# Performance work log

Measured on AMD Instinct MI355X. Metric: run time of the kernel, lower is better.

The kernel has to match this reference:

```python
import jax, jax.numpy as jnp
import numpy as np

B, V, C, M, CM, D, OUT = 16, 16, 64, 32, 16, 128, 600
VOCAB = {"cond": 4000, "proc": 2000, "drug": 600, "lab_item": 700, "lab_value": 2000, "inj_item": 400, "inj_value": 2000}


def _gru(x, Wih, Whh, bih, bhh):
    """Batch-first torch-style GRU. x: [N,T,D] -> (outputs [N,T,D], h_T [N,D])."""
    Dh = Whh.shape[1]

    def step(h, xt):
        gi = xt @ Wih.T + bih
        gh = h @ Whh.T + bhh
        ir, iz, ig = jnp.split(gi, 3, axis=-1)
        hr, hz, hg = jnp.split(gh, 3, axis=-1)
        r = jax.nn.sigmoid(ir + hr)
        z = jax.nn.sigmoid(iz + hz)
        n = jnp.tanh(ig + r * hg)
        h = (1.0 - z) * n + z * h
        return h, h

    h0 = jnp.zeros((x.shape[0], Dh), x.dtype)
    hT, ys = jax.lax.scan(step, h0, jnp.swapaxes(x, 0, 1))
    return jnp.swapaxes(ys, 0, 1), hT


def _hetero_mp(feats, Wself, Wmsg):
    """Heterogeneous message passing over node types on the fully-connected
    monitor<->visit-feature bipartite pattern: each node type combines a self
    transform with a transformed mean of the other node types, then ReLU.
    feats: list of [N,D]; Wself/Wmsg: [T,D,D]."""
    stacked = jnp.stack(feats)  # [T,N,D]
    total = jnp.sum(stacked, axis=0)
    T = stacked.shape[0]
    outs = []
    for t in range(T):
        others = (total - stacked[t]) / (T - 1)
        outs.append(jax.nn.relu(stacked[t] @ Wself[t] + others @ Wmsg[t]))
    return outs


def _forward(codes_cond, codes_proc, codes_drug, codes_lab_item, codes_lab_value,
             codes_inj_item, codes_inj_value, weight, age,
             emb_cond, emb_proc, emb_drug, emb_lab_item, emb_lab_value,
             emb_inj_item, emb_inj_value,
             mgru_Wih, mgru_Whh, mgru_bih, mgru_bhh,
             vgru_Wih, vgru_Whh, vgru_bih, vgru_bhh,
             gnn_Wself, gnn_Wmsg,
             fc_weight_W, fc_weight_b, fc_age_W, fc_age_b,
             fc_patient_W, fc_patient_b):
    # ---- visit-event features: embedding lookup + sum-pool over codes ----
    vis = {}
    for k, codes, emb in (("cond", codes_cond, emb_cond),
                          ("proc", codes_proc, emb_proc),
                          ("drug", codes_drug, emb_drug)):
        vis[k] = jnp.sum(emb[codes], axis=2)  # [B,V,D]
    visit_keys = ("cond", "proc", "drug")

    # ---- monitor-event pairs: (item * value) embeddings, GNN, two-level GRU ----
    pairs = (
        (codes_lab_item, codes_lab_value, emb_lab_item, emb_lab_value, "lab_item", (0, 2, 3, 4)),
        (codes_inj_item, codes_inj_value, emb_inj_item, emb_inj_value, "inj_item", (1, 2, 3, 4)),
    )
    hid = {}
    for p, (ci, cv, ei, ev, ikey, gidx) in enumerate(pairs):
        mon = jnp.sum(ei[ci] * ev[cv], axis=3)  # [B,V,M,D]
        feats = [mon.reshape(-1, D)]  # monitor node type, [B*V*M, D]
        for k in visit_keys:  # visit features repeated across monitors
            feats.append(jnp.broadcast_to(vis[k][:, :, None, :], (B, V, M, D)).reshape(-1, D))
        outs = _hetero_mp(feats, gnn_Wself[p], gnn_Wmsg[p])
        for t, k in enumerate((ikey,) + visit_keys):
            g = gidx[t]
            # monitor-level GRU over the M monitors of each visit
            o, _ = _gru(outs[t].reshape(B * V, M, D), mgru_Wih[g], mgru_Whh[g], mgru_bih[g], mgru_bhh[g])
            last = o[:, -1, :].reshape(B, V, D)  # last monitor state per visit
            # visit-level GRU (source uses visit_gru[feature_key1] for all keys)
            _, h = _gru(last, vgru_Wih[p], vgru_Whh[p], vgru_bih[p], vgru_bhh[p])
            hid[k] = h if k not in hid else hid[k] + h

    # ---- weight / age scalar features ----
    for k, x, W, b, vi in (("weight", weight, fc_weight_W, fc_weight_b, 2),
                           ("age", age, fc_age_W, fc_age_b, 3)):
        mask = (x != 0.0)[..., None]  # [B,V,1]
        xe = (x[..., None] * W[:, 0] + b) * mask  # Linear(1->D) then zero-mask
        _, h = _gru(xe, vgru_Wih[vi], vgru_Whh[vi], vgru_bih[vi], vgru_bhh[vi])
        hid[k] = h

    # ---- concat in dict-insertion order, then ReLU + Linear head ----
    pe = jnp.concatenate([hid["lab_item"], hid["cond"], hid["proc"], hid["drug"],
                          hid["inj_item"], hid["weight"], hid["age"]], axis=-1)  # [B, 7D]
    return jax.nn.relu(pe) @ fc_patient_W.T + fc_patient_b  # [B, OUT]


def setup_inputs() -> dict:
    key = jax.random.key(0)
    ks = iter(jax.random.split(key, 64))

    def nrm(shape, s=0.1):
        return (jax.random.normal(next(ks), shape) * s).astype(jnp.float32)

    def emb_table(vsz):
        t = nrm((vsz, D), 1.0)
        return t.at[0].set(0.0)  # padding_idx=0 row is zero

    inp = {}
    inp["codes_cond"] = jax.random.randint(next(ks), (B, V, C), 0, VOCAB["cond"], dtype=jnp.int32)
    inp["codes_proc"] = jax.random.randint(next(ks), (B, V, C), 0, VOCAB["proc"], dtype=jnp.int32)
    inp["codes_drug"] = jax.random.randint(next(ks), (B, V, C), 0, VOCAB["drug"], dtype=jnp.int32)
    inp["codes_lab_item"] = jax.random.randint(next(ks), (B, V, M, CM), 0, VOCAB["lab_item"], dtype=jnp.int32)
    inp["codes_lab_value"] = jax.random.randint(next(ks), (B, V, M, CM), 0, VOCAB["lab_value"], dtype=jnp.int32)
    inp["codes_inj_item"] = jax.random.randint(next(ks), (B, V, M, CM), 0, VOCAB["inj_item"], dtype=jnp.int32)
    inp["codes_inj_value"] = jax.random.randint(next(ks), (B, V, M, CM), 0, VOCAB["inj_value"], dtype=jnp.int32)
    inp["weight"] = jax.random.uniform(next(ks), (B, V), minval=0.1, maxval=1.0, dtype=jnp.float32)
    inp["age"] = jax.random.uniform(next(ks), (B, V), minval=0.1, maxval=1.0, dtype=jnp.float32)
    inp["emb_cond"] = emb_table(VOCAB["cond"])
    inp["emb_proc"] = emb_table(VOCAB["proc"])
    inp["emb_drug"] = emb_table(VOCAB["drug"])
    inp["emb_lab_item"] = emb_table(VOCAB["lab_item"])
    inp["emb_lab_value"] = emb_table(VOCAB["lab_value"])
    inp["emb_inj_item"] = emb_table(VOCAB["inj_item"])
    inp["emb_inj_value"] = emb_table(VOCAB["inj_value"])
    inp["mgru_Wih"] = nrm((5, 3 * D, D))
    inp["mgru_Whh"] = nrm((5, 3 * D, D))
    inp["mgru_bih"] = nrm((5, 3 * D))
    inp["mgru_bhh"] = nrm((5, 3 * D))
    inp["vgru_Wih"] = nrm((4, 3 * D, D))
    inp["vgru_Whh"] = nrm((4, 3 * D, D))
    inp["vgru_bih"] = nrm((4, 3 * D))
    inp["vgru_bhh"] = nrm((4, 3 * D))
    inp["gnn_Wself"] = nrm((2, 4, D, D))
    inp["gnn_Wmsg"] = nrm((2, 4, D, D))
    inp["fc_weight_W"] = nrm((D, 1))
    inp["fc_weight_b"] = nrm((D,))
    inp["fc_age_W"] = nrm((D, 1))
    inp["fc_age_b"] = nrm((D,))
    inp["fc_patient_W"] = nrm((OUT, 7 * D))
    inp["fc_patient_b"] = nrm((OUT,))
    return inp


def reference(codes_cond, codes_proc, codes_drug, codes_lab_item, codes_lab_value,
              codes_inj_item, codes_inj_value, weight, age,
              emb_cond, emb_proc, emb_drug, emb_lab_item, emb_lab_value,
              emb_inj_item, emb_inj_value,
              mgru_Wih, mgru_Whh, mgru_bih, mgru_bhh,
              vgru_Wih, vgru_Whh, vgru_bih, vgru_bhh,
              gnn_Wself, gnn_Wmsg,
              fc_weight_W, fc_weight_b, fc_age_W, fc_age_b,
              fc_patient_W, fc_patient_b):
    return _forward(codes_cond, codes_proc, codes_drug, codes_lab_item, codes_lab_value,
                    codes_inj_item, codes_inj_value, weight, age,
                    emb_cond, emb_proc, emb_drug, emb_lab_item, emb_lab_value,
                    emb_inj_item, emb_inj_value,
                    mgru_Wih, mgru_Whh, mgru_bih, mgru_bhh,
                    vgru_Wih, vgru_Whh, vgru_bih, vgru_bhh,
                    gnn_Wself, gnn_Wmsg,
                    fc_weight_W, fc_weight_b, fc_age_W, fc_age_b,
                    fc_patient_W, fc_patient_b)
```

## Files before the change

kernel.cpp:

```cpp
#include <hip/hip_runtime.h>
#include <math.h>

#define B_   16
#define V_   16
#define C_   64
#define M_   32
#define CM_  16
#define D_   128
#define OUT_ 600
#define NSEQ 256
#define NROW 8192

typedef __attribute__((ext_vector_type(8))) short bf16x8;
typedef __attribute__((ext_vector_type(4))) short bf16x4;
typedef __attribute__((ext_vector_type(4))) float f32x4;

__device__ __forceinline__ unsigned short f2bf(float x) {
  union { float f; unsigned u; } v; v.f = x;
  unsigned r = v.u + 0x7fff + ((v.u >> 16) & 1);
  return (unsigned short)(r >> 16);
}
__device__ __forceinline__ float bf2f(short s) {
  union { unsigned u; float f; } v;
  v.u = ((unsigned)(unsigned short)s) << 16;
  return v.f;
}
__device__ __forceinline__ float fsig(float x)  { return __fdividef(1.f, 1.f + __expf(-x)); }
__device__ __forceinline__ float ftanh(float x) { return 1.f - 2.f*__fdividef(1.f, __expf(2.f*x) + 1.f); }

constexpr int OFF_VIS   = 0;
constexpr int OFF_VISB  = 98304;
constexpr int OFF_MONB  = 147456;
constexpr int OFF_TOTB  = 1196032;
constexpr int OFF_W12T  = 2244608;
constexpr int OFF_WIHB  = 2375680;
constexpr int OFF_WIHTV = 2498560;
constexpr int OFF_XE    = 2695168;
constexpr int OFF_GI    = 2760704;
constexpr int OFF_LAST  = 27926528;
constexpr int OFF_VGI   = 28188672;
constexpr int OFF_VH    = 29171712;
constexpr int OFF_PE    = 29192192;

__global__ __launch_bounds__(256) void k_prep(
    const float* __restrict__ Wself, const float* __restrict__ Wmsg,
    const float* __restrict__ mWih,  const float* __restrict__ vWih,
    const float* __restrict__ wgt,   const float* __restrict__ age,
    const float* __restrict__ fwW,   const float* __restrict__ fwB,
    const float* __restrict__ faW,   const float* __restrict__ faB,
    short* __restrict__ w12t, short* __restrict__ wihb,
    float* __restrict__ wihTv, float* __restrict__ xe)
{
  int bx = blockIdx.x, tid = threadIdx.x;
  if (bx < 1024) {
    int lin = bx*256 + tid;
    int pt = lin >> 15, rem = lin & 32767;
    int n = rem >> 8, k = rem & 255;
    float v;
    if (k < 128) v = Wself[pt*16384 + k*128 + n] - Wmsg[pt*16384 + k*128 + n]*(1.f/3.f);
    else         v = Wmsg[pt*16384 + (k-128)*128 + n]*(1.f/3.f);
    w12t[lin] = (short)f2bf(v);
  } else if (bx < 1984) {
    int lin = (bx-1024)*256 + tid;
    wihb[lin] = (short)f2bf(mWih[lin]);
  } else if (bx < 2752) {
    int lin = (bx-1984)*256 + tid;
    int g = lin / 49152, rem2 = lin % 49152;
    int k = rem2 / 384, j = rem2 % 384;
    wihTv[lin] = vWih[g*49152 + j*128 + k];
  } else {
    int lin = (bx-2752)*256 + tid;
    int which = lin >> 15, rem2 = lin & 32767;
    int n = rem2 >> 7, d = rem2 & 127;
    float x  = which ? age[n] : wgt[n];
    float Wv = which ? faW[d] : fwW[d];
    float bb = which ? faB[d] : fwB[d];
    xe[lin] = (x != 0.0f) ? (x*Wv + bb) : 0.0f;
  }
}

__global__ __launch_bounds__(128) void k_vis(
    const int* __restrict__ cc, const int* __restrict__ cp, const int* __restrict__ cd,
    const float* __restrict__ ec, const float* __restrict__ ep, const float* __restrict__ ed,
    float* __restrict__ vis, short* __restrict__ visb)
{
  int type = blockIdx.x >> 8;
  int bv   = blockIdx.x & 255;
  int d    = threadIdx.x;
  const int*   codes = (type==0) ? cc : (type==1) ? cp : cd;
  const float* emb   = (type==0) ? ec : (type==1) ? ep : ed;
  float acc = 0.f;
  for (int c = 0; c < C_; ++c) {
    int code = codes[bv*C_ + c];
    acc += emb[code*D_ + d];
  }
  vis [(type*NSEQ + bv)*D_ + d] = acc;
  visb[(type*NSEQ + bv)*D_ + d] = (short)f2bf(acc);
}

__global__ __launch_bounds__(128) void k_mon(
    const int* __restrict__ cli, const int* __restrict__ clv,
    const int* __restrict__ cii, const int* __restrict__ civ,
    const float* __restrict__ eli, const float* __restrict__ elv,
    const float* __restrict__ eii, const float* __restrict__ eiv,
    const float* __restrict__ vis,
    short* __restrict__ monb, short* __restrict__ totb)
{
  int p   = blockIdx.x >> 13;
  int bvm = blockIdx.x & 8191;
  int d   = threadIdx.x;
  const int* ci = p ? cii : cli;  const int* cv = p ? civ : clv;
  const float* ei = p ? eii : eli; const float* ev = p ? eiv : elv;
  float acc = 0.f;
  #pragma unroll
  for (int c = 0; c < CM_; ++c) {
    int iv = ci[bvm*CM_ + c];
    int vv = cv[bvm*CM_ + c];
    acc += ei[iv*D_ + d] * ev[vv*D_ + d];
  }
  int bv = bvm >> 5;
  float vsum = vis[bv*D_ + d] + vis[(NSEQ + bv)*D_ + d] + vis[(2*NSEQ + bv)*D_ + d];
  monb[(p*NROW + bvm)*D_ + d] = (short)f2bf(acc);
  totb[(p*NROW + bvm)*D_ + d] = (short)f2bf(acc + vsum);
}

__global__ __launch_bounds__(256, 4) void k_gg(
    const short* __restrict__ monb, const short* __restrict__ totb,
    const short* __restrict__ visb, const short* __restrict__ w12t,
    const short* __restrict__ wihb, const float* __restrict__ mbih,
    short* __restrict__ gi)
{
  const int pt = blockIdx.x >> 6;
  const int rb = blockIdx.x & 63;
  const int p = pt >> 2, t = pt & 3;
  const int g = (pt % 4 == 0) ? (pt / 4) : (pt % 4 + 1);
  const int row0 = rb * 128;
  const int tid = threadIdx.x;
  const int w = tid >> 6, lane = tid & 63;
  const int c = lane & 15, q = lane >> 4;

  __shared__ short smem[2*128*72];
  short (*Xs)[72]  = (short(*)[72])smem;
  short (*Ws)[72]  = (short(*)[72])(smem + 128*72);
  short (*Ys)[136] = (short(*)[136])smem;
  float (*giS)[68] = (float(*)[68])smem;

  const int rowL = tid >> 1, kc = tid & 1;
  const int rowG = row0 + rowL;
  const int bv = rowG >> 5;
  const int mg = w >> 1, ng = w & 1;

  f32x4 acc1[4][4];
  #pragma unroll
  for (int mi = 0; mi < 4; ++mi)
    #pragma unroll
    for (int ni = 0; ni < 4; ++ni) acc1[mi][ni] = (f32x4){0.f,0.f,0.f,0.f};

  const short* featp = (t == 0) ? (monb + ((size_t)p*NROW + rowG)*128)
                                : (visb + ((size_t)(t-1)*NSEQ + bv)*128);
  const short* totp  = totb + ((size_t)p*NROW + rowG)*128;
  const short* wrow  = w12t + ((size_t)pt*128 + rowL)*256;

  #pragma unroll 1
  for (int ks = 0; ks < 4; ++ks) {
    __syncthreads();
    int kg = ks*64 + kc*32;
    const short* srcX = (kg < 128) ? (featp + kg) : (totp + (kg - 128));
    const short* srcW = wrow + kg;
    short* dX = &Xs[rowL][kc*32];
    short* dW = &Ws[rowL][kc*32];
    #pragma unroll
    for (int i = 0; i < 4; ++i) {
      *(bf16x8*)(dX + 8*i) = *(const bf16x8*)(srcX + 8*i);
      *(bf16x8*)(dW + 8*i) = *(const bf16x8*)(srcW + 8*i);
    }
    __syncthreads();
    #pragma unroll
    for (int kk = 0; kk < 2; ++kk) {
      bf16x8 af[4], bfr[4];
      #pragma unroll
      for (int mi = 0; mi < 4; ++mi)
        af[mi] = *(const bf16x8*)&Xs[(mg*4+mi)*16 + c][kk*32 + q*8];
      #pragma unroll
      for (int ni = 0; ni < 4; ++ni)
        bfr[ni] = *(const bf16x8*)&Ws[(ng*4+ni)*16 + c][kk*32 + q*8];
      #pragma unroll
      for (int mi = 0; mi < 4; ++mi)
        #pragma unroll
        for (int ni = 0; ni < 4; ++ni)
          acc1[mi][ni] = __builtin_amdgcn_mfma_f32_16x16x32_bf16(af[mi], bfr[ni], acc1[mi][ni], 0, 0, 0);
    }
  }
  __syncthreads();

  #pragma unroll
  for (int mi = 0; mi < 4; ++mi)
    #pragma unroll
    for (int ni = 0; ni < 4; ++ni)
      #pragma unroll
      for (int reg = 0; reg < 4; ++reg)
        Ys[(mg*4+mi)*16 + q*4 + reg][(ng*4+ni)*16 + c] =
            (short)f2bf(fmaxf(acc1[mi][ni][reg], 0.f));
  __syncthreads();

  bf16x8 Af[2][4];
  #pragma unroll
  for (int mi = 0; mi < 2; ++mi)
    #pragma unroll
    for (int kt = 0; kt < 4; ++kt)
      Af[mi][kt] = *(const bf16x8*)&Ys[(w*2+mi)*16 + c][kt*32 + q*8];

  float bihv[24];
  #pragma unroll
  for (int nt = 0; nt < 24; ++nt)
    bihv[nt] = mbih[g*384 + nt*16 + c];

  short* gslab = gi + (((size_t)pt*64 + rb)*32)*384*4;
  #pragma unroll 1
  for (int cn = 0; cn < 6; ++cn) {
    f32x4 acc2[2][4];
    #pragma unroll
    for (int mi = 0; mi < 2; ++mi)
      #pragma unroll
      for (int ni = 0; ni < 4; ++ni) acc2[mi][ni] = (f32x4){0.f,0.f,0.f,0.f};
    #pragma unroll
    for (int ni = 0; ni < 4; ++ni) {
      int n = (cn*4 + ni)*16 + c;
      const short* bp_ = wihb + ((size_t)g*384 + n)*128 + q*8;
      #pragma unroll
      for (int kt = 0; kt < 4; ++kt) {
        bf16x8 bfr = *(const bf16x8*)(bp_ + kt*32);
        #pragma unroll
        for (int mi = 0; mi < 2; ++mi)
          acc2[mi][ni] = __builtin_amdgcn_mfma_f32_16x16x32_bf16(Af[mi][kt], bfr, acc2[mi][ni], 0, 0, 0);
      }
    }
    __syncthreads();
    #pragma unroll
    for (int mi = 0; mi < 2; ++mi)
      #pragma unroll
      for (int ni = 0; ni < 4; ++ni) {
        float bia = bihv[cn*4+ni];
        #pragma unroll
        for (int reg = 0; reg < 4; ++reg)
          giS[(w*2+mi)*16 + q*4 + reg][ni*16 + c] = acc2[mi][ni][reg] + bia;
      }
    __syncthreads();
    #pragma unroll
    for (int k = 0; k < 8; ++k) {
      int o4 = tid + k*256;
      int m = o4 >> 6, colL = o4 & 63;
      bf16x4 v;
      v[0] = (short)f2bf(giS[m][colL]);
      v[1] = (short)f2bf(giS[32+m][colL]);
      v[2] = (short)f2bf(giS[64+m][colL]);
      v[3] = (short)f2bf(giS[96+m][colL]);
      *(bf16x4*)&gslab[((size_t)m*384 + cn*64 + colL)*4] = v;
    }
  }
}

__global__ __launch_bounds__(512, 1) void k_mgru(
    const short* __restrict__ gi, const float* __restrict__ mWhh,
    const float* __restrict__ mbhh, float* __restrict__ last)
{
  const int run = blockIdx.x >> 5, grp = blockIdx.x & 31;
  const int g = (run % 4 == 0) ? (run / 4) : (run % 4 + 1);
  const int tid = threadIdx.x;
  const int w = tid >> 6;
  const int lane = tid & 63;
  const int c = lane & 15, q = lane >> 4;

  __shared__ short hb[2][4][16][40];
  for (int idx = tid; idx < 2*4*16*40; idx += 512)
    ((short*)hb)[idx] = 0;

  const int jh = w*16 + c;

  bf16x8 bfrag[3][4];
  #pragma unroll
  for (int gate = 0; gate < 3; ++gate) {
    const float* wp = mWhh + ((size_t)g*384 + gate*128 + jh)*128 + q*8;
    #pragma unroll
    for (int kt = 0; kt < 4; ++kt) {
      float4 lo = *(const float4*)(wp + kt*32);
      float4 hi = *(const float4*)(wp + kt*32 + 4);
      bf16x8 t;
      t[0]=(short)f2bf(lo.x); t[1]=(short)f2bf(lo.y); t[2]=(short)f2bf(lo.z); t[3]=(short)f2bf(lo.w);
      t[4]=(short)f2bf(hi.x); t[5]=(short)f2bf(hi.y); t[6]=(short)f2bf(hi.z); t[7]=(short)f2bf(hi.w);
      bfrag[gate][kt] = t;
    }
  }
  float bh_[3];
  #pragma unroll
  for (int gate = 0; gate < 3; ++gate)
    bh_[gate] = mbhh[g*384 + gate*128 + jh];

  float hf[4] = {0.f,0.f,0.f,0.f};
  const short* gib = gi + (((size_t)run*64 + grp*2 + q)*32)*384*4;
  const bool act = (lane < 32);

  bf16x4 gA[3], gB[3];
  if (act) {
    #pragma unroll
    for (int gate = 0; gate < 3; ++gate)
      gA[gate] = *(const bf16x4*)&gib[(size_t)(0*384 + gate*128 + jh)*4];
  }
  __syncthreads();

  auto dostep = [&](int m, bf16x4 (&gcur)[3], bf16x4 (&gnext)[3]) {
    const int cur = m & 1, nxt = cur ^ 1;
    bf16x8 a[4];
    #pragma unroll
    for (int kt = 0; kt < 4; ++kt)
      a[kt] = *(const bf16x8*)&hb[cur][kt][c][q*8];

    f32x4 acc[3];
    #pragma unroll
    for (int gate = 0; gate < 3; ++gate) {
      f32x4 t = {0.f,0.f,0.f,0.f};
      #pragma unroll
      for (int kt = 0; kt < 4; ++kt)
        t = __builtin_amdgcn_mfma_f32_16x16x32_bf16(a[kt], bfrag[gate][kt], t, 0, 0, 0);
      acc[gate] = t;
    }

    if (act && m < 31) {
      #pragma unroll
      for (int gate = 0; gate < 3; ++gate)
        gnext[gate] = *(const bf16x4*)&gib[(size_t)((m+1)*384 + gate*128 + jh)*4];
    }

    if (act) {
      const int kt = jh >> 5, kk = jh & 31;
      #pragma unroll
      for (int reg = 0; reg < 4; ++reg) {
        int row = q*4 + reg;
        float g0 = bf2f(gcur[0][reg]);
        float g1 = bf2f(gcur[1][reg]);
        float g2 = bf2f(gcur[2][reg]);
        float rr = fsig(acc[0][reg] + bh_[0] + g0);
        float zz = fsig(acc[1][reg] + bh_[1] + g1);
        float nn = ftanh(g2 + rr*(acc[2][reg] + bh_[2]));
        float hnew = (1.f - zz)*nn + zz*hf[reg];
        hf[reg] = hnew;
        hb[nxt][kt][row][kk] = (short)f2bf(hnew);
      }
    }
    __syncthreads();
  };

  #pragma unroll 1
  for (int m2 = 0; m2 < 16; ++m2) {
    dostep(2*m2,     gA, gB);
    dostep(2*m2 + 1, gB, gA);
  }

  if (act) {
    #pragma unroll
    for (int reg = 0; reg < 4; ++reg)
      last[(run*NSEQ + grp*8 + q*4 + reg)*D_ + jh] = hf[reg];
  }
}

__global__ __launch_bounds__(384) void k_vgi(
    const float* __restrict__ last, const float* __restrict__ xe,
    const float* __restrict__ wihTv, const float* __restrict__ vbih,
    float* __restrict__ vgi)
{
  int run = blockIdx.x >> 5;
  int rblk = blockIdx.x & 31;
  int j = threadIdx.x;
  int vidx = (run < 4) ? 0 : (run < 8) ? 1 : (run - 6);
  __shared__ float Xs[8][128];
  const float* X = (run < 8) ? (last + run*NSEQ*D_) : (xe + (run-8)*NSEQ*D_);
  for (int idx = j; idx < 1024; idx += 384) {
    int s = idx >> 7, k = idx & 127;
    Xs[s][k] = X[(rblk*8 + s)*D_ + k];
  }
  __syncthreads();
  float acc[8];
  float bias = vbih[vidx*384 + j];
  #pragma unroll
  for (int s = 0; s < 8; ++s) acc[s] = bias;
  const float* W = wihTv + vidx*49152 + j;
  #pragma unroll 4
  for (int k = 0; k < 128; ++k) {
    float wv = W[k*384];
    #pragma unroll
    for (int s = 0; s < 8; ++s) acc[s] += Xs[s][k] * wv;
  }
  #pragma unroll
  for (int s = 0; s < 8; ++s)
    vgi[(run*NSEQ + rblk*8 + s)*384 + j] = acc[s];
}

__global__ __launch_bounds__(768) void k_vgru(
    const float* __restrict__ vgi, const float* __restrict__ vWhh,
    const float* __restrict__ vbhh, float* __restrict__ vh)
{
  int run = blockIdx.x >> 4, b = blockIdx.x & 15;
  int tid = threadIdx.x;
  int j = tid >> 1, kh = tid & 1;
  int vidx = (run < 4) ? 0 : (run < 8) ? 1 : (run - 6);
  float w[64];
  const float4* wrow = (const float4*)(vWhh + (vidx*384 + j)*128 + kh*64);
  #pragma unroll
  for (int k4 = 0; k4 < 16; ++k4) {
    float4 t4 = wrow[k4];
    w[4*k4] = t4.x; w[4*k4+1] = t4.y; w[4*k4+2] = t4.z; w[4*k4+3] = t4.w;
  }
  float bj = vbhh[vidx*384 + j];
  __shared__ __align__(16) float hsv[128];
  __shared__ float gh[384];
  if (tid < 128) hsv[tid] = 0.f;
  __syncthreads();
  const float* gib = vgi + (run*NSEQ + b*16)*384;
  #pragma unroll 1
  for (int v = 0; v < 16; ++v) {
    const float4* h4 = (const float4*)(hsv + kh*64);
    float p0 = 0.f, p1 = 0.f;
    #pragma unroll
    for (int k4 = 0; k4 < 8; ++k4) {
      float4 u0 = h4[k4], u1 = h4[k4+8];
      p0 += w[4*k4   ]*u0.x + w[4*k4+1 ]*u0.y + w[4*k4+2 ]*u0.z + w[4*k4+3 ]*u0.w;
      p1 += w[4*k4+32]*u1.x + w[4*k4+33]*u1.y + w[4*k4+34]*u1.z + w[4*k4+35]*u1.w;
    }
    float part = p0 + p1;
    part += __shfl_xor(part, 1);
    if (kh == 0) gh[j] = bj + ((j < 256) ? gib[v*384 + j] : 0.f) + part;
    __syncthreads();
    if (tid < 128) {
      float r = fsig(gh[tid]);
      float z = fsig(gh[tid+128]);
      float gin = gib[v*384 + 256 + tid];
      float n = ftanh(gin + r*gh[tid+256]);
      hsv[tid] = (1.f - z)*n + z*hsv[tid];
    }
    __syncthreads();
  }
  if (tid < 128) vh[(run*16 + b)*D_ + tid] = hsv[tid];
}

__global__ __launch_bounds__(256) void k_pe(
    const float* __restrict__ vh, float* __restrict__ pe)
{
  int idx = blockIdx.x*256 + threadIdx.x;
  int b = idx / 896, cc2 = idx % 896;
  int s = cc2 >> 7, d = cc2 & 127;
  const int a1[7] = {0,1,2,3,4,8,9};
  const int a2[7] = {-1,5,6,7,-1,-1,-1};
  float v = vh[(a1[s]*16 + b)*D_ + d];
  int s2 = a2[s];
  if (s2 >= 0) v += vh[(s2*16 + b)*D_ + d];
  pe[idx] = fmaxf(v, 0.f);
}

__global__ __launch_bounds__(256) void k_head(
    const float* __restrict__ pe, const float* __restrict__ Wp,
    const float* __restrict__ bp, float* __restrict__ out)
{
  const int o = blockIdx.x;
  const int tid = threadIdx.x;
  const int b = tid & 15, kc = tid >> 4;
  const float4* pb = (const float4*)(pe + b*896 + kc*56);
  const float4* wb = (const float4*)(Wp + (size_t)o*896 + kc*56);
  float acc = 0.f;
  #pragma unroll
  for (int i = 0; i < 14; ++i) {
    float4 a = pb[i], w = wb[i];
    acc += a.x*w.x + a.y*w.y + a.z*w.z + a.w*w.w;
  }
  __shared__ float red[16][17];
  red[kc][b] = acc;
  __syncthreads();
  if (tid < 16) {
    float s = 0.f;
    #pragma unroll
    for (int k = 0; k < 16; ++k) s += red[k][tid];
    out[tid*OUT_ + o] = s + bp[o];
  }
}

extern "C" void kernel_launch(void* const* d_in, const int* in_sizes, int n_in,
                              void* d_out, int out_size, void* d_ws, size_t ws_size,
                              hipStream_t stream)
{
  (void)in_sizes; (void)n_in; (void)out_size; (void)ws_size;
  const int*   cc   = (const int*)  d_in[0];
  const int*   cp   = (const int*)  d_in[1];
  const int*   cd   = (const int*)  d_in[2];
  const int*   cli  = (const int*)  d_in[3];
  const int*   clv  = (const int*)  d_in[4];
  const int*   cii  = (const int*)  d_in[5];
  const int*   civ  = (const int*)  d_in[6];
  const float* wgt  = (const float*)d_in[7];
  const float* age  = (const float*)d_in[8];
  const float* ec   = (const float*)d_in[9];
  const float* ep   = (const float*)d_in[10];
  const float* ed   = (const float*)d_in[11];
  const float* eli  = (const float*)d_in[12];
  const float* elv  = (const float*)d_in[13];
  const float* eii  = (const float*)d_in[14];
  const float* eiv  = (const float*)d_in[15];
  const float* mWih = (const float*)d_in[16];
  const float* mWhh = (const float*)d_in[17];
  const float* mbih = (const float*)d_in[18];
  const float* mbhh = (const float*)d_in[19];
  const float* vWih = (const float*)d_in[20];
  const float* vWhh = (const float*)d_in[21];
  const float* vbih = (const float*)d_in[22];
  const float* vbhh = (const float*)d_in[23];
  const float* Wself= (const float*)d_in[24];
  const float* Wmsg = (const float*)d_in[25];
  const float* fwW  = (const float*)d_in[26];
  const float* fwB  = (const float*)d_in[27];
  const float* faW  = (const float*)d_in[28];
  const float* faB  = (const float*)d_in[29];
  const float* Wp   = (const float*)d_in[30];
  const float* bp   = (const float*)d_in[31];
  float* out = (float*)d_out;
  float* ws  = (float*)d_ws;

  float* vis   = ws + OFF_VIS;
  short* visb  = (short*)(ws + OFF_VISB);
  short* monb  = (short*)(ws + OFF_MONB);
  short* totb  = (short*)(ws + OFF_TOTB);
  short* w12t  = (short*)(ws + OFF_W12T);
  short* wihb  = (short*)(ws + OFF_WIHB);
  float* wihTv = ws + OFF_WIHTV;
  float* xe    = ws + OFF_XE;
  short* gi    = (short*)(ws + OFF_GI);
  float* last  = ws + OFF_LAST;
  float* vgi   = ws + OFF_VGI;
  float* vh    = ws + OFF_VH;
  float* pe    = ws + OFF_PE;

  k_prep<<<3008, 256, 0, stream>>>(Wself, Wmsg, mWih, vWih, wgt, age,
                                   fwW, fwB, faW, faB, w12t, wihb, wihTv, xe);
  k_vis <<<768, 128, 0, stream>>>(cc, cp, cd, ec, ep, ed, vis, visb);
  k_mon <<<16384, 128, 0, stream>>>(cli, clv, cii, civ, eli, elv, eii, eiv,
                                    vis, monb, totb);
  k_gg  <<<512, 256, 0, stream>>>(monb, totb, visb, w12t, wihb, mbih, gi);
  k_mgru<<<256, 512, 0, stream>>>(gi, mWhh, mbhh, last);
  k_vgi <<<320, 384, 0, stream>>>(last, xe, wihTv, vbih, vgi);
  k_vgru<<<160, 768, 0, stream>>>(vgi, vWhh, vbhh, vh);
  k_pe  <<<56, 256, 0, stream>>>(vh, pe);
  k_head<<<600, 256, 0, stream>>>(pe, Wp, bp, out);
}
```

Baseline: 285.1 us.

## Fuse vis into prep, input projection into vgru, and pe into head

Merges the visit embedding pooling into the weight-prep kernel as extra blocks, computes the visit GRU input projection inside the GRU kernel into shared memory, and folds the patient-embedding ReLU/sum into the head GEMV. This cuts three kernel launches and the global round-trips for vgi and pe. In exchange, the GRU kernel uses much more shared memory and redundantly reads wihTv per block. The head kernel also recomputes the pe values once per output column.

```diff
diff --git a/kernel.cpp b/kernel.cpp
--- a/kernel.cpp
+++ b/kernel.cpp
@@ -38,18 +38,19 @@
 constexpr int OFF_XE    = 2695168;
 constexpr int OFF_GI    = 2760704;
 constexpr int OFF_LAST  = 27926528;
-constexpr int OFF_VGI   = 28188672;
 constexpr int OFF_VH    = 29171712;
-constexpr int OFF_PE    = 29192192;
-
-__global__ __launch_bounds__(256) void k_prep(
+
+__global__ __launch_bounds__(256) void k_prepvis(
     const float* __restrict__ Wself, const float* __restrict__ Wmsg,
     const float* __restrict__ mWih,  const float* __restrict__ vWih,
     const float* __restrict__ wgt,   const float* __restrict__ age,
     const float* __restrict__ fwW,   const float* __restrict__ fwB,
     const float* __restrict__ faW,   const float* __restrict__ faB,
+    const int* __restrict__ cc, const int* __restrict__ cp, const int* __restrict__ cd,
+    const float* __restrict__ ec, const float* __restrict__ ep, const float* __restrict__ ed,
     short* __restrict__ w12t, short* __restrict__ wihb,
-    float* __restrict__ wihTv, float* __restrict__ xe)
+    float* __restrict__ wihTv, float* __restrict__ xe,
+    float* __restrict__ vis, short* __restrict__ visb)
 {
   int bx = blockIdx.x, tid = threadIdx.x;
   if (bx < 1024) {
@@ -68,7 +69,7 @@
     int g = lin / 49152, rem2 = lin % 49152;
     int k = rem2 / 384, j = rem2 % 384;
     wihTv[lin] = vWih[g*49152 + j*128 + k];
-  } else {
+  } else if (bx < 3008) {
     int lin = (bx-2752)*256 + tid;
     int which = lin >> 15, rem2 = lin & 32767;
     int n = rem2 >> 7, d = rem2 & 127;
@@ -76,26 +77,21 @@
     float Wv = which ? faW[d] : fwW[d];
     float bb = which ? faB[d] : fwB[d];
     xe[lin] = (x != 0.0f) ? (x*Wv + bb) : 0.0f;
-  }
-}
-
-__global__ __launch_bounds__(128) void k_vis(
-    const int* __restrict__ cc, const int* __restrict__ cp, const int* __restrict__ cd,
-    const float* __restrict__ ec, const float* __restrict__ ep, const float* __restrict__ ed,
-    float* __restrict__ vis, short* __restrict__ visb)
-{
-  int type = blockIdx.x >> 8;
-  int bv   = blockIdx.x & 255;
-  int d    = threadIdx.x;
-  const int*   codes = (type==0) ? cc : (type==1) ? cp : cd;
-  const float* emb   = (type==0) ? ec : (type==1) ? ep : ed;
-  float acc = 0.f;
-  for (int c = 0; c < C_; ++c) {
-    int code = codes[bv*C_ + c];
-    acc += emb[code*D_ + d];
-  }
-  vis [(type*NSEQ + bv)*D_ + d] = acc;
-  visb[(type*NSEQ + bv)*D_ + d] = (short)f2bf(acc);
+  } else {
+    int idx = (bx-3008)*256 + tid;
+    int type = idx >> 15;
+    int r = idx & 32767;
+    int bv = r >> 7, d = r & 127;
+    const int*   codes = (type==0) ? cc : (type==1) ? cp : cd;
+    const float* emb   = (type==0) ? ec : (type==1) ? ep : ed;
+    float acc = 0.f;
+    for (int c = 0; c < C_; ++c) {
+      int code = codes[bv*C_ + c];
+      acc += emb[code*D_ + d];
+    }
+    vis [(type*NSEQ + bv)*D_ + d] = acc;
+    visb[(type*NSEQ + bv)*D_ + d] = (short)f2bf(acc);
+  }
 }
 
 __global__ __launch_bounds__(128) void k_mon(
@@ -363,46 +359,48 @@
   }
 }
 
-__global__ __launch_bounds__(384) void k_vgi(
+__global__ __launch_bounds__(768) void k_vgru(
     const float* __restrict__ last, const float* __restrict__ xe,
     const float* __restrict__ wihTv, const float* __restrict__ vbih,
-    float* __restrict__ vgi)
-{
-  int run = blockIdx.x >> 5;
-  int rblk = blockIdx.x & 31;
-  int j = threadIdx.x;
-  int vidx = (run < 4) ? 0 : (run < 8) ? 1 : (run - 6);
-  __shared__ float Xs[8][128];
-  const float* X = (run < 8) ? (last + run*NSEQ*D_) : (xe + (run-8)*NSEQ*D_);
-  for (int idx = j; idx < 1024; idx += 384) {
-    int s = idx >> 7, k = idx & 127;
-    Xs[s][k] = X[(rblk*8 + s)*D_ + k];
-  }
-  __syncthreads();
-  float acc[8];
-  float bias = vbih[vidx*384 + j];
-  #pragma unroll
-  for (int s = 0; s < 8; ++s) acc[s] = bias;
-  const float* W = wihTv + vidx*49152 + j;
-  #pragma unroll 4
-  for (int k = 0; k < 128; ++k) {
-    float wv = W[k*384];
-    #pragma unroll
-    for (int s = 0; s < 8; ++s) acc[s] += Xs[s][k] * wv;
-  }
-  #pragma unroll
-  for (int s = 0; s < 8; ++s)
-    vgi[(run*NSEQ + rblk*8 + s)*384 + j] = acc[s];
-}
-
-__global__ __launch_bounds__(768) void k_vgru(
-    const float* __restrict__ vgi, const float* __restrict__ vWhh,
-    const float* __restrict__ vbhh, float* __restrict__ vh)
+    const float* __restrict__ vWhh, const float* __restrict__ vbhh,
+    float* __restrict__ vh)
 {
   int run = blockIdx.x >> 4, b = blockIdx.x & 15;
   int tid = threadIdx.x;
+  int vidx = (run < 4) ? 0 : (run < 8) ? 1 : (run - 6);
+
+  __shared__ float Xs[16][128];
+  __shared__ float giL[16*384];
+  __shared__ __align__(16) float hsv[128];
+  __shared__ float gh[384];
+
+  const float* X = (run < 8) ? (last + ((size_t)run*NSEQ + b*16)*D_)
+                             : (xe + ((size_t)(run-8)*NSEQ + b*16)*D_);
+  for (int idx = tid; idx < 2048; idx += 768)
+    ((float*)Xs)[idx] = X[idx];
+  if (tid < 128) hsv[tid] = 0.f;
+  __syncthreads();
+
+  {
+    int half = (tid >= 384) ? 1 : 0;
+    int j = tid - half*384;
+    float accv[8];
+    float bias = vbih[vidx*384 + j];
+    #pragma unroll
+    for (int s = 0; s < 8; ++s) accv[s] = bias;
+    const float* W = wihTv + vidx*49152 + j;
+    #pragma unroll 4
+    for (int k = 0; k < 128; ++k) {
+      float wv = W[k*384];
+      #pragma unroll
+      for (int s = 0; s < 8; ++s) accv[s] += Xs[half*8 + s][k] * wv;
+    }
+    #pragma unroll
+    for (int s = 0; s < 8; ++s)
+      giL[(half*8 + s)*384 + j] = accv[s];
+  }
+
   int j = tid >> 1, kh = tid & 1;
-  int vidx = (run < 4) ? 0 : (run < 8) ? 1 : (run - 6);
   float w[64];
   const float4* wrow = (const float4*)(vWhh + (vidx*384 + j)*128 + kh*64);
   #pragma unroll
@@ -411,11 +409,8 @@
     w[4*k4] = t4.x; w[4*k4+1] = t4.y; w[4*k4+2] = t4.z; w[4*k4+3] = t4.w;
   }
   float bj = vbhh[vidx*384 + j];
-  __shared__ __align__(16) float hsv[128];
-  __shared__ float gh[384];
-  if (tid < 128) hsv[tid] = 0.f;
   __syncthreads();
-  const float* gib = vgi + (run*NSEQ + b*16)*384;
+
   #pragma unroll 1
   for (int v = 0; v < 16; ++v) {
     const float4* h4 = (const float4*)(hsv + kh*64);
@@ -428,12 +423,12 @@
     }
     float part = p0 + p1;
     part += __shfl_xor(part, 1);
-    if (kh == 0) gh[j] = bj + ((j < 256) ? gib[v*384 + j] : 0.f) + part;
+    if (kh == 0) gh[j] = bj + ((j < 256) ? giL[v*384 + j] : 0.f) + part;
     __syncthreads();
     if (tid < 128) {
       float r = fsig(gh[tid]);
       float z = fsig(gh[tid+128]);
-      float gin = gib[v*384 + 256 + tid];
+      float gin = giL[v*384 + 256 + tid];
       float n = ftanh(gin + r*gh[tid+256]);
       hsv[tid] = (1.f - z)*n + z*hsv[tid];
     }
@@ -442,34 +437,31 @@
   if (tid < 128) vh[(run*16 + b)*D_ + tid] = hsv[tid];
 }
 
-__global__ __launch_bounds__(256) void k_pe(
-    const float* __restrict__ vh, float* __restrict__ pe)
-{
-  int idx = blockIdx.x*256 + threadIdx.x;
-  int b = idx / 896, cc2 = idx % 896;
-  int s = cc2 >> 7, d = cc2 & 127;
-  const int a1[7] = {0,1,2,3,4,8,9};
-  const int a2[7] = {-1,5,6,7,-1,-1,-1};
-  float v = vh[(a1[s]*16 + b)*D_ + d];
-  int s2 = a2[s];
-  if (s2 >= 0) v += vh[(s2*16 + b)*D_ + d];
-  pe[idx] = fmaxf(v, 0.f);
-}
-
 __global__ __launch_bounds__(256) void k_head(
-    const float* __restrict__ pe, const float* __restrict__ Wp,
+    const float* __restrict__ vh, const float* __restrict__ Wp,
     const float* __restrict__ bp, float* __restrict__ out)
 {
   const int o = blockIdx.x;
   const int tid = threadIdx.x;
   const int b = tid & 15, kc = tid >> 4;
-  const float4* pb = (const float4*)(pe + b*896 + kc*56);
+  const int a1[7] = {0,1,2,3,4,8,9};
+  const int a2[7] = {-1,5,6,7,-1,-1,-1};
   const float4* wb = (const float4*)(Wp + (size_t)o*896 + kc*56);
   float acc = 0.f;
   #pragma unroll
   for (int i = 0; i < 14; ++i) {
-    float4 a = pb[i], w = wb[i];
-    acc += a.x*w.x + a.y*w.y + a.z*w.z + a.w*w.w;
+    int cc2 = kc*56 + i*4;
+    int s = cc2 >> 7, d0 = cc2 & 127;
+    float4 a = *(const float4*)(vh + (a1[s]*16 + b)*D_ + d0);
+    int s2 = a2[s];
+    if (s2 >= 0) {
+      float4 a2v = *(const float4*)(vh + (s2*16 + b)*D_ + d0);
+      a.x += a2v.x; a.y += a2v.y; a.z += a2v.z; a.w += a2v.w;
+    }
+    a.x = fmaxf(a.x, 0.f); a.y = fmaxf(a.y, 0.f);
+    a.z = fmaxf(a.z, 0.f); a.w = fmaxf(a.w, 0.f);
+    float4 ww = wb[i];
+    acc += a.x*ww.x + a.y*ww.y + a.z*ww.z + a.w*ww.w;
   }
   __shared__ float red[16][17];
   red[kc][b] = acc;
@@ -532,19 +524,16 @@
   float* xe    = ws + OFF_XE;
   short* gi    = (short*)(ws + OFF_GI);
   float* last  = ws + OFF_LAST;
-  float* vgi   = ws + OFF_VGI;
   float* vh    = ws + OFF_VH;
-  float* pe    = ws + OFF_PE;
-
-  k_prep<<<3008, 256, 0, stream>>>(Wself, Wmsg, mWih, vWih, wgt, age,
-                                   fwW, fwB, faW, faB, w12t, wihb, wihTv, xe);
-  k_vis <<<768, 128, 0, stream>>>(cc, cp, cd, ec, ep, ed, vis, visb);
+
+  k_prepvis<<<3392, 256, 0, stream>>>(Wself, Wmsg, mWih, vWih, wgt, age,
+                                      fwW, fwB, faW, faB,
+                                      cc, cp, cd, ec, ep, ed,
+                                      w12t, wihb, wihTv, xe, vis, visb);
   k_mon <<<16384, 128, 0, stream>>>(cli, clv, cii, civ, eli, elv, eii, eiv,
                                     vis, monb, totb);
   k_gg  <<<512, 256, 0, stream>>>(monb, totb, visb, w12t, wihb, mbih, gi);
   k_mgru<<<256, 512, 0, stream>>>(gi, mWhh, mbhh, last);
-  k_vgi <<<320, 384, 0, stream>>>(last, xe, wihTv, vbih, vgi);
-  k_vgru<<<160, 768, 0, stream>>>(vgi, vWhh, vbhh, vh);
-  k_pe  <<<56, 256, 0, stream>>>(vh, pe);
-  k_head<<<600, 256, 0, stream>>>(pe, Wp, bp, out);
-}
+  k_vgru<<<160, 768, 0, stream>>>(last, xe, wihTv, vbih, vWhh, vbhh, vh);
+  k_head<<<600, 256, 0, stream>>>(vh, Wp, bp, out);
+}
```

Result: faster. 276.7 us, median of 3 (-2.9%).
